# Performance work log

Measured on AMD Instinct MI355X. Metric: run time of the kernel, lower is better.

Reference implementation:

```python
import jax, jax.numpy as jnp
import numpy as np
from jax import lax

B, T, IN, H = 4096, 512, 11, 16


def lstm(x, Wih, Whh, bih, bhh):
    # x: [B, T, in]; PyTorch gate order i, f, g, o packed along 4H.
    xg = jnp.einsum('bti,gi->btg', x, Wih) + bih + bhh  # [B, T, 4H]
    h0 = jnp.zeros((x.shape[0], Whh.shape[1]), x.dtype)
    c0 = jnp.zeros_like(h0)

    def step(carry, xg_t):
        h, c = carry
        g = xg_t + h @ Whh.T                      # [B, 4H]
        i, f, gg, o = jnp.split(g, 4, axis=-1)
        i = jax.nn.sigmoid(i)
        f = jax.nn.sigmoid(f)
        gg = jnp.tanh(gg)
        o = jax.nn.sigmoid(o)
        c = f * c + i * gg
        h = o * jnp.tanh(c)
        return (h, c), h

    _, hs = lax.scan(step, (h0, c0), jnp.swapaxes(xg, 0, 1))  # hs: [T, B, H]
    return jnp.swapaxes(hs, 0, 1)  # [B, T, H]


def setup_inputs() -> dict:
    key = jax.random.key(0)
    ks = jax.random.split(key, 16)
    s = 1.0 / np.sqrt(H)
    u = lambda k, shape: jax.random.uniform(k, shape, jnp.float32, -s, s)
    return {
        'x': jax.random.normal(ks[0], (B, T, IN), jnp.float32),
        'Wih1': u(ks[1], (4 * H, IN)), 'Whh1': u(ks[2], (4 * H, H)),
        'bih1': u(ks[3], (4 * H,)), 'bhh1': u(ks[4], (4 * H,)),
        'Wih2': u(ks[5], (4 * H, H)), 'Whh2': u(ks[6], (4 * H, H)),
        'bih2': u(ks[7], (4 * H,)), 'bhh2': u(ks[8], (4 * H,)),
        'Wd1': u(ks[9], (8, H)), 'bd1': u(ks[10], (8,)),
        'Wd2': u(ks[11], (8, 8)), 'bd2': u(ks[12], (8,)),
        'Wd3': u(ks[13], (3, 8)), 'bd3': u(ks[14], (3,)),
    }


def reference(x, Wih1, Whh1, bih1, bhh1, Wih2, Whh2, bih2, bhh2,
              Wd1, bd1, Wd2, bd2, Wd3, bd3):
    h1 = lstm(x, Wih1, Whh1, bih1, bhh1)          # [B, T, H]
    # Dropout2d treated as identity (eval mode).
    h2 = lstm(h1, Wih2, Whh2, bih2, bhh2)          # [B, T, H]
    s = jax.nn.softmax(h2, axis=1)[:, -1, :]       # softmax over TIME, take last step -> [B, H]
    d = (s @ Wd1.T + bd1) @ Wd2.T + bd2
    d = d @ Wd3.T + bd3                            # [B, 3]
    return jax.nn.softmax(d, axis=1)
```

## Files before the change

### kernel.cpp

```cpp
#include <hip/hip_runtime.h>

#define T_STEPS 512
#define IN_DIM 11
#define ROW_PAD 12
#define H_DIM 16
#define ROW_F (T_STEPS * IN_DIM)
#define CHUNK_T 16
#define CHUNK_F (CHUNK_T * IN_DIM)
#define N_CHUNK (T_STEPS / CHUNK_T)
#define LOG2E 1.44269504088896340736f

typedef float v2f __attribute__((ext_vector_type(2)));
typedef float v4f __attribute__((ext_vector_type(4)));

__device__ __forceinline__ v2f pk_fma(v2f a, v2f b, v2f c) {
    v2f d;
    asm("v_pk_fma_f32 %0, %1, %2, %3" : "=v"(d) : "v"(a), "v"(b), "v"(c));
    return d;
}

template<int CTRL>
__device__ __forceinline__ float qperm(float v) {
    return __builtin_bit_cast(float,
        __builtin_amdgcn_update_dpp(0, __builtin_bit_cast(int, v),
                                    CTRL, 0xf, 0xf, true));
}

__device__ __forceinline__ float bcast_lane(float v, int l) {
    return __builtin_bit_cast(float,
        __builtin_amdgcn_readlane(__builtin_bit_cast(int, v), l));
}

__global__ __launch_bounds__(256, 4) void lstm2_head(
    const float* __restrict__ x,
    const float* __restrict__ Wih1, const float* __restrict__ Whh1,
    const float* __restrict__ bih1, const float* __restrict__ bhh1,
    const float* __restrict__ Wih2, const float* __restrict__ Whh2,
    const float* __restrict__ bih2, const float* __restrict__ bhh2,
    const float* __restrict__ Wd1, const float* __restrict__ bd1,
    const float* __restrict__ Wd2, const float* __restrict__ bd2,
    const float* __restrict__ Wd3, const float* __restrict__ bd3,
    float* __restrict__ out)
{
    __shared__ alignas(16) float xlds[2][212];
    __shared__ alignas(16) float ring[2][2][CHUNK_T][H_DIM];
    __shared__ alignas(16) float shh2[2][H_DIM];

    const int lane = threadIdx.x & 63;
    const int wid = __builtin_amdgcn_readfirstlane((int)(threadIdx.x >> 6));
    const int isL2 = wid >> 1;
    const int bw   = wid & 1;
    const int b    = blockIdx.x * 2 + bw;

    const int r   = lane >> 2;
    const int gt  = lane & 3;
    const int row = gt * H_DIM + r;

    const bool is_t = (gt == 2);
    const float M   = is_t ? (-2.0f * LOG2E) : (-LOG2E);
    const float vAa = is_t ? 2.0f : 1.0f;
    const float vBc = is_t ? -1.0f : 0.0f;

    v2f win[8], wrec[8];
    float bb;
    if (!isL2) {
        #pragma unroll
        for (int j = 0; j < 5; ++j)
            win[j] = (v2f){M * Wih1[row * IN_DIM + 2 * j],
                           M * Wih1[row * IN_DIM + 2 * j + 1]};
        win[5] = (v2f){M * Wih1[row * IN_DIM + 10], 0.0f};
        win[6] = (v2f){0.f, 0.f};
        win[7] = (v2f){0.f, 0.f};
        #pragma unroll
        for (int j = 0; j < 8; ++j)
            wrec[j] = (v2f){M * Whh1[row * H_DIM + 2 * j],
                            M * Whh1[row * H_DIM + 2 * j + 1]};
        bb = M * (bih1[row] + bhh1[row]);
    } else {
        #pragma unroll
        for (int j = 0; j < 8; ++j) {
            win[j]  = (v2f){M * Wih2[row * H_DIM + 2 * j],
                            M * Wih2[row * H_DIM + 2 * j + 1]};
            wrec[j] = (v2f){M * Whh2[row * H_DIM + 2 * j],
                            M * Whh2[row * H_DIM + 2 * j + 1]};
        }
        bb = M * (bih2[row] + bhh2[row]);
    }
    #pragma unroll
    for (int j = 0; j < 8; ++j) {
        asm volatile("" : "+v"(win[j]));
        asm volatile("" : "+v"(wrec[j]));
    }

    const int f1i = lane, f2i = lane + 64, f3i = lane + 128;
    const int p1 = (f1i / IN_DIM) * ROW_PAD + (f1i % IN_DIM);
    const int p2 = (f2i / IN_DIM) * ROW_PAD + (f2i % IN_DIM);
    const int p3 = (f3i / IN_DIM) * ROW_PAD + (f3i % IN_DIM);
    const float* __restrict__ xb = x + (size_t)b * ROW_F;

    float gl0 = 0.f, gl1 = 0.f, gl2 = 0.f;
    if (!isL2) {
        if (lane < 16) xlds[bw][lane * ROW_PAD + IN_DIM] = 0.0f;
        gl0 = xb[f1i];
        gl1 = xb[f2i];
        gl2 = xb[min(f3i, ROW_F - 1)];
    }

    float cst = 0.f, ssum = 0.f, h2v = 0.f;
    v2f hr[8];
    #pragma unroll
    for (int j = 0; j < 8; ++j) hr[j] = (v2f){0.f, 0.f};

    for (int ck = 0; ck <= N_CHUNK; ++ck) {
        __syncthreads();

        if (!isL2) {
            if (ck < N_CHUNK) {
                float* const xbuf = &xlds[bw][0];
                xbuf[p1] = gl0;
                xbuf[p2] = gl1;
                xbuf[p3] = gl2;
                if (ck + 1 < N_CHUNK) {
                    const int base = (ck + 1) * CHUNK_F;
                    gl0 = xb[base + f1i];
                    gl1 = xb[base + f2i];
                    gl2 = xb[min(base + f3i, ROW_F - 1)];
                }
                float (* const rg)[H_DIM] = ring[bw][ck & 1];
                #pragma unroll
                for (int t2 = 0; t2 < CHUNK_T; ++t2) {
                    const v2f* const xr = (const v2f*)(xbuf + t2 * ROW_PAD);
                    v2f ap = pk_fma(win[0], xr[0], (v2f){bb, 0.f});
                    v2f aq = pk_fma(win[1], xr[1], (v2f){0.f, 0.f});
                    ap = pk_fma(win[2], xr[2], ap);
                    aq = pk_fma(win[3], xr[3], aq);
                    ap = pk_fma(win[4], xr[4], ap);
                    aq = pk_fma(win[5], xr[5], aq);
                    #pragma unroll
                    for (int j = 0; j < 8; j += 2) {
                        ap = pk_fma(wrec[j],     hr[j],     ap);
                        aq = pk_fma(wrec[j + 1], hr[j + 1], aq);
                    }
                    const v2f s = ap + aq;
                    const float g = s.x + s.y;
                    const float a = __builtin_fmaf(vAa,
                        __builtin_amdgcn_rcpf(1.0f + __builtin_amdgcn_exp2f(g)), vBc);
                    const float gi = qperm<0x00>(a);
                    const float gf = qperm<0x55>(a);
                    const float gg = qperm<0xAA>(a);
                    const float go = qperm<0xFF>(a);
                    cst = __builtin_fmaf(gf, cst, gi * gg);
                    const float tc = __builtin_fmaf(2.0f,
                        __builtin_amdgcn_rcpf(1.0f +
                            __builtin_amdgcn_exp2f(-2.0f * LOG2E * cst)), -1.0f);
                    rg[t2][r] = go * tc;
                    const v4f* const hq = (const v4f*)&rg[t2][0];
                    #pragma unroll
                    for (int j = 0; j < 4; ++j) {
                        const v4f q = hq[j];
                        hr[2 * j]     = (v2f){q.x, q.y};
                        hr[2 * j + 1] = (v2f){q.z, q.w};
                    }
                }
            }
        } else {
            if (ck >= 1) {
                float (* const rg)[H_DIM] = ring[bw][(ck - 1) & 1];
                #pragma unroll
                for (int t2 = 0; t2 < CHUNK_T; ++t2) {
                    const v4f* const hq = (const v4f*)&rg[t2][0];
                    const v4f q0 = hq[0];
                    const v4f q1 = hq[1];
                    v2f ap = pk_fma(wrec[0], hr[0], (v2f){bb, 0.f});
                    v2f aq = pk_fma(wrec[1], hr[1], (v2f){0.f, 0.f});
                    #pragma unroll
                    for (int j = 2; j < 8; j += 2) {
                        ap = pk_fma(wrec[j],     hr[j],     ap);
                        aq = pk_fma(wrec[j + 1], hr[j + 1], aq);
                    }
                    ap = pk_fma(win[0], (v2f){q0.x, q0.y}, ap);
                    aq = pk_fma(win[1], (v2f){q0.z, q0.w}, aq);
                    const v4f q2 = hq[2];
                    const v4f q3 = hq[3];
                    ap = pk_fma(win[2], (v2f){q1.x, q1.y}, ap);
                    aq = pk_fma(win[3], (v2f){q1.z, q1.w}, aq);
                    ap = pk_fma(win[4], (v2f){q2.x, q2.y}, ap);
                    aq = pk_fma(win[5], (v2f){q2.z, q2.w}, aq);
                    ap = pk_fma(win[6], (v2f){q3.x, q3.y}, ap);
                    aq = pk_fma(win[7], (v2f){q3.z, q3.w}, aq);
                    const v2f s = ap + aq;
                    const float g = s.x + s.y;
                    const float a = __builtin_fmaf(vAa,
                        __builtin_amdgcn_rcpf(1.0f + __builtin_amdgcn_exp2f(g)), vBc);
                    const float gi = qperm<0x00>(a);
                    const float gf = qperm<0x55>(a);
                    const float gg = qperm<0xAA>(a);
                    const float go = qperm<0xFF>(a);
                    cst = __builtin_fmaf(gf, cst, gi * gg);
                    const float tc = __builtin_fmaf(2.0f,
                        __builtin_amdgcn_rcpf(1.0f +
                            __builtin_amdgcn_exp2f(-2.0f * LOG2E * cst)), -1.0f);
                    h2v = go * tc;
                    shh2[bw][r] = h2v;
                    const v4f* const h2q = (const v4f*)&shh2[bw][0];
                    #pragma unroll
                    for (int j = 0; j < 4; ++j) {
                        const v4f q = h2q[j];
                        hr[2 * j]     = (v2f){q.x, q.y};
                        hr[2 * j + 1] = (v2f){q.z, q.w};
                    }
                    ssum += __builtin_amdgcn_exp2f(LOG2E * h2v);
                }
            }
        }
    }

    if (isL2) {
        const float sv = __builtin_amdgcn_exp2f(LOG2E * h2v) / ssum;

        float ssb[H_DIM];
        #pragma unroll
        for (int k = 0; k < H_DIM; ++k) ssb[k] = bcast_lane(sv, 4 * k);

        const int r8 = lane & 7;
        float acc1 = bd1[r8];
        #pragma unroll
        for (int k = 0; k < H_DIM; ++k)
            acc1 = __builtin_fmaf(Wd1[r8 * H_DIM + k], ssb[k], acc1);

        float d1s[8];
        #pragma unroll
        for (int j = 0; j < 8; ++j) d1s[j] = bcast_lane(acc1, j);

        float acc2 = bd2[r8];
        #pragma unroll
        for (int k = 0; k < 8; ++k)
            acc2 = __builtin_fmaf(Wd2[r8 * 8 + k], d1s[k], acc2);

        float d2s[8];
        #pragma unroll
        for (int j = 0; j < 8; ++j) d2s[j] = bcast_lane(acc2, j);

        float lg = 0.f;
        if (lane < 3) {
            lg = bd3[lane];
            #pragma unroll
            for (int k = 0; k < 8; ++k)
                lg = __builtin_fmaf(Wd3[lane * 8 + k], d2s[k], lg);
        }
        const float l0 = bcast_lane(lg, 0);
        const float l1 = bcast_lane(lg, 1);
        const float l2 = bcast_lane(lg, 2);
        const float mx = fmaxf(l0, fmaxf(l1, l2));
        const float e0 = __builtin_amdgcn_exp2f(LOG2E * (l0 - mx));
        const float e1 = __builtin_amdgcn_exp2f(LOG2E * (l1 - mx));
        const float e2 = __builtin_amdgcn_exp2f(LOG2E * (l2 - mx));
        const float inv = 1.0f / (e0 + e1 + e2);
        if (lane < 3) {
            const float ev = (lane == 0) ? e0 : ((lane == 1) ? e1 : e2);
            out[b * 3 + lane] = ev * inv;
        }
    }
}

extern "C" void kernel_launch(void* const* d_in, const int* in_sizes, int n_in,
                              void* d_out, int out_size, void* d_ws, size_t ws_size,
                              hipStream_t stream) {
    (void)in_sizes; (void)n_in; (void)out_size; (void)d_ws; (void)ws_size;
    const float* x    = (const float*)d_in[0];
    const float* Wih1 = (const float*)d_in[1];
    const float* Whh1 = (const float*)d_in[2];
    const float* bih1 = (const float*)d_in[3];
    const float* bhh1 = (const float*)d_in[4];
    const float* Wih2 = (const float*)d_in[5];
    const float* Whh2 = (const float*)d_in[6];
    const float* bih2 = (const float*)d_in[7];
    const float* bhh2 = (const float*)d_in[8];
    const float* Wd1  = (const float*)d_in[9];
    const float* bd1  = (const float*)d_in[10];
    const float* Wd2  = (const float*)d_in[11];
    const float* bd2  = (const float*)d_in[12];
    const float* Wd3  = (const float*)d_in[13];
    const float* bd3  = (const float*)d_in[14];

    lstm2_head<<<dim3(4096 / 2), dim3(256), 0, stream>>>(
        x, Wih1, Whh1, bih1, bhh1, Wih2, Whh2, bih2, bhh2,
        Wd1, bd1, Wd2, bd2, Wd3, bd3, (float*)d_out);
}
```

Baseline: 495.2 us.

## Exchange recurrent hidden state via ds_swizzle and bpermute instead of LDS round-trip

Replaces the per-step LDS write and broadcast read of the hidden state with a distributed recurrent matvec. Each lane now holds pre-permuted Whh weights, gathers its neighbours' h values with ds_swizzle, and combines partial sums from other lane groups with ds_bpermute. The input projection is computed off the critical path and added to the recurrent result afterwards. The goal is a shorter serial dependency chain per timestep. In exchange it adds cross-lane permute latency and relies on subtle lane-index arithmetic being correct.

```diff
diff --git a/kernel.cpp b/kernel.cpp
--- a/kernel.cpp
+++ b/kernel.cpp
@@ -30,6 +30,54 @@
     return __builtin_bit_cast(float,
         __builtin_amdgcn_readlane(__builtin_bit_cast(int, v), l));
 }
+
+template<int PAT>
+__device__ __forceinline__ float swz(float v) {
+    return __builtin_bit_cast(float,
+        __builtin_amdgcn_ds_swizzle(__builtin_bit_cast(int, v), PAT));
+}
+
+__device__ __forceinline__ float bperm(int addr, float v) {
+    return __builtin_bit_cast(float,
+        __builtin_amdgcn_ds_bpermute(addr, __builtin_bit_cast(int, v)));
+}
+
+__device__ __forceinline__ float rec_dot(float hv,
+        const v2f wq0[2], const v2f wq1[2], const v2f wq2[2], const v2f wq3[2],
+        float bias, int a16, int a32, int a48) {
+    const float g1 = swz<0x101F>(hv);
+    const float g2 = swz<0x201F>(hv);
+    const float g3 = swz<0x301F>(hv);
+    const v2f hp0 = (v2f){hv, g1};
+    const v2f hp1 = (v2f){g2, g3};
+    v2f d0 = pk_fma(wq0[0], hp0, (v2f){bias, 0.f});
+    d0 = pk_fma(wq0[1], hp1, d0);
+    v2f d1 = pk_fma(wq1[0], hp0, (v2f){0.f, 0.f});
+    d1 = pk_fma(wq1[1], hp1, d1);
+    v2f d2 = pk_fma(wq2[0], hp0, (v2f){0.f, 0.f});
+    d2 = pk_fma(wq2[1], hp1, d2);
+    v2f d3 = pk_fma(wq3[0], hp0, (v2f){0.f, 0.f});
+    d3 = pk_fma(wq3[1], hp1, d3);
+    const float r1 = bperm(a16, d1.x + d1.y);
+    const float r2 = bperm(a32, d2.x + d2.y);
+    const float r3 = bperm(a48, d3.x + d3.y);
+    return (d0.x + d0.y) + r1 + r2 + r3;
+}
+
+#define ACT_STEP(gsum, cst, hv_out)                                           \
+    {                                                                         \
+        const float a_ = __builtin_fmaf(vAa,                                  \
+            __builtin_amdgcn_rcpf(1.0f + __builtin_amdgcn_exp2f(gsum)), vBc); \
+        const float gi_ = qperm<0x00>(a_);                                    \
+        const float gf_ = qperm<0x55>(a_);                                    \
+        const float gg_ = qperm<0xAA>(a_);                                    \
+        const float go_ = qperm<0xFF>(a_);                                    \
+        cst = __builtin_fmaf(gf_, cst, gi_ * gg_);                            \
+        const float tc_ = __builtin_fmaf(2.0f,                                \
+            __builtin_amdgcn_rcpf(1.0f +                                      \
+                __builtin_amdgcn_exp2f(-2.0f * LOG2E * cst)), -1.0f);         \
+        hv_out = go_ * tc_;                                                   \
+    }
 
 __global__ __launch_bounds__(256, 4) void lstm2_head(
     const float* __restrict__ x,
@@ -44,7 +92,6 @@
 {
     __shared__ alignas(16) float xlds[2][212];
     __shared__ alignas(16) float ring[2][2][CHUNK_T][H_DIM];
-    __shared__ alignas(16) float shh2[2][H_DIM];
 
     const int lane = threadIdx.x & 63;
     const int wid = __builtin_amdgcn_readfirstlane((int)(threadIdx.x >> 6));
@@ -55,13 +102,34 @@
     const int r   = lane >> 2;
     const int gt  = lane & 3;
     const int row = gt * H_DIM + r;
+    const int q     = r & 3;
+    const int rbase = r & 12;
 
     const bool is_t = (gt == 2);
     const float M   = is_t ? (-2.0f * LOG2E) : (-LOG2E);
     const float vAa = is_t ? 2.0f : 1.0f;
     const float vBc = is_t ? -1.0f : 0.0f;
 
-    v2f win[8], wrec[8];
+    const int idx0 = r;
+    const int idx1 = rbase | (q ^ 1);
+    const int idx2 = rbase | (q ^ 2);
+    const int idx3 = rbase | (q ^ 3);
+    const int rowP1 = gt * H_DIM + (r ^ 4);
+    const int rowP2 = gt * H_DIM + (r ^ 8);
+    const int rowP3 = gt * H_DIM + (r ^ 12);
+
+    const float* __restrict__ Wrec = isL2 ? Whh2 : Whh1;
+    v2f wq0[2], wq1[2], wq2[2], wq3[2];
+    wq0[0] = (v2f){M * Wrec[row  * H_DIM + idx0], M * Wrec[row  * H_DIM + idx1]};
+    wq0[1] = (v2f){M * Wrec[row  * H_DIM + idx2], M * Wrec[row  * H_DIM + idx3]};
+    wq1[0] = (v2f){M * Wrec[rowP1 * H_DIM + idx0], M * Wrec[rowP1 * H_DIM + idx1]};
+    wq1[1] = (v2f){M * Wrec[rowP1 * H_DIM + idx2], M * Wrec[rowP1 * H_DIM + idx3]};
+    wq2[0] = (v2f){M * Wrec[rowP2 * H_DIM + idx0], M * Wrec[rowP2 * H_DIM + idx1]};
+    wq2[1] = (v2f){M * Wrec[rowP2 * H_DIM + idx2], M * Wrec[rowP2 * H_DIM + idx3]};
+    wq3[0] = (v2f){M * Wrec[rowP3 * H_DIM + idx0], M * Wrec[rowP3 * H_DIM + idx1]};
+    wq3[1] = (v2f){M * Wrec[rowP3 * H_DIM + idx2], M * Wrec[rowP3 * H_DIM + idx3]};
+
+    v2f win[8];
     float bb;
     if (!isL2) {
         #pragma unroll
@@ -71,26 +139,27 @@
         win[5] = (v2f){M * Wih1[row * IN_DIM + 10], 0.0f};
         win[6] = (v2f){0.f, 0.f};
         win[7] = (v2f){0.f, 0.f};
-        #pragma unroll
-        for (int j = 0; j < 8; ++j)
-            wrec[j] = (v2f){M * Whh1[row * H_DIM + 2 * j],
-                            M * Whh1[row * H_DIM + 2 * j + 1]};
         bb = M * (bih1[row] + bhh1[row]);
     } else {
         #pragma unroll
-        for (int j = 0; j < 8; ++j) {
-            win[j]  = (v2f){M * Wih2[row * H_DIM + 2 * j],
-                            M * Wih2[row * H_DIM + 2 * j + 1]};
-            wrec[j] = (v2f){M * Whh2[row * H_DIM + 2 * j],
-                            M * Whh2[row * H_DIM + 2 * j + 1]};
-        }
+        for (int j = 0; j < 8; ++j)
+            win[j] = (v2f){M * Wih2[row * H_DIM + 2 * j],
+                           M * Wih2[row * H_DIM + 2 * j + 1]};
         bb = M * (bih2[row] + bhh2[row]);
     }
     #pragma unroll
-    for (int j = 0; j < 8; ++j) {
-        asm volatile("" : "+v"(win[j]));
-        asm volatile("" : "+v"(wrec[j]));
-    }
+    for (int j = 0; j < 8; ++j) asm volatile("" : "+v"(win[j]));
+    #pragma unroll
+    for (int j = 0; j < 2; ++j) {
+        asm volatile("" : "+v"(wq0[j]));
+        asm volatile("" : "+v"(wq1[j]));
+        asm volatile("" : "+v"(wq2[j]));
+        asm volatile("" : "+v"(wq3[j]));
+    }
+
+    const int a16 = (lane ^ 16) << 2;
+    const int a32 = (lane ^ 32) << 2;
+    const int a48 = (lane ^ 48) << 2;
 
     const int f1i = lane, f2i = lane + 64, f3i = lane + 128;
     const int p1 = (f1i / IN_DIM) * ROW_PAD + (f1i % IN_DIM);
@@ -106,10 +175,7 @@
         gl2 = xb[min(f3i, ROW_F - 1)];
     }
 
-    float cst = 0.f, ssum = 0.f, h2v = 0.f;
-    v2f hr[8];
-    #pragma unroll
-    for (int j = 0; j < 8; ++j) hr[j] = (v2f){0.f, 0.f};
+    float cst = 0.f, ssum = 0.f, hv = 0.f;
 
     for (int ck = 0; ck <= N_CHUNK; ++ck) {
         __syncthreads();
@@ -129,38 +195,18 @@
                 float (* const rg)[H_DIM] = ring[bw][ck & 1];
                 #pragma unroll
                 for (int t2 = 0; t2 < CHUNK_T; ++t2) {
+                    const float rec = rec_dot(hv, wq0, wq1, wq2, wq3, bb,
+                                              a16, a32, a48);
                     const v2f* const xr = (const v2f*)(xbuf + t2 * ROW_PAD);
-                    v2f ap = pk_fma(win[0], xr[0], (v2f){bb, 0.f});
-                    v2f aq = pk_fma(win[1], xr[1], (v2f){0.f, 0.f});
-                    ap = pk_fma(win[2], xr[2], ap);
-                    aq = pk_fma(win[3], xr[3], aq);
-                    ap = pk_fma(win[4], xr[4], ap);
-                    aq = pk_fma(win[5], xr[5], aq);
-                    #pragma unroll
-                    for (int j = 0; j < 8; j += 2) {
-                        ap = pk_fma(wrec[j],     hr[j],     ap);
-                        aq = pk_fma(wrec[j + 1], hr[j + 1], aq);
-                    }
-                    const v2f s = ap + aq;
-                    const float g = s.x + s.y;
-                    const float a = __builtin_fmaf(vAa,
-                        __builtin_amdgcn_rcpf(1.0f + __builtin_amdgcn_exp2f(g)), vBc);
-                    const float gi = qperm<0x00>(a);
-                    const float gf = qperm<0x55>(a);
-                    const float gg = qperm<0xAA>(a);
-                    const float go = qperm<0xFF>(a);
-                    cst = __builtin_fmaf(gf, cst, gi * gg);
-                    const float tc = __builtin_fmaf(2.0f,
-                        __builtin_amdgcn_rcpf(1.0f +
-                            __builtin_amdgcn_exp2f(-2.0f * LOG2E * cst)), -1.0f);
-                    rg[t2][r] = go * tc;
-                    const v4f* const hq = (const v4f*)&rg[t2][0];
-                    #pragma unroll
-                    for (int j = 0; j < 4; ++j) {
-                        const v4f q = hq[j];
-                        hr[2 * j]     = (v2f){q.x, q.y};
-                        hr[2 * j + 1] = (v2f){q.z, q.w};
-                    }
+                    v2f xa = pk_fma(win[0], xr[0], (v2f){0.f, 0.f});
+                    v2f xc = pk_fma(win[1], xr[1], (v2f){0.f, 0.f});
+                    xa = pk_fma(win[2], xr[2], xa);
+                    xc = pk_fma(win[3], xr[3], xc);
+                    xa = pk_fma(win[4], xr[4], xa);
+                    xc = pk_fma(win[5], xr[5], xc);
+                    const float g = rec + (xa.x + xa.y) + (xc.x + xc.y);
+                    ACT_STEP(g, cst, hv);
+                    rg[t2][r] = hv;
                 }
             }
         } else {
@@ -168,55 +214,31 @@
                 float (* const rg)[H_DIM] = ring[bw][(ck - 1) & 1];
                 #pragma unroll
                 for (int t2 = 0; t2 < CHUNK_T; ++t2) {
+                    const float rec = rec_dot(hv, wq0, wq1, wq2, wq3, bb,
+                                              a16, a32, a48);
                     const v4f* const hq = (const v4f*)&rg[t2][0];
                     const v4f q0 = hq[0];
                     const v4f q1 = hq[1];
-                    v2f ap = pk_fma(wrec[0], hr[0], (v2f){bb, 0.f});
-                    v2f aq = pk_fma(wrec[1], hr[1], (v2f){0.f, 0.f});
-                    #pragma unroll
-                    for (int j = 2; j < 8; j += 2) {
-                        ap = pk_fma(wrec[j],     hr[j],     ap);
-                        aq = pk_fma(wrec[j + 1], hr[j + 1], aq);
-                    }
-                    ap = pk_fma(win[0], (v2f){q0.x, q0.y}, ap);
-                    aq = pk_fma(win[1], (v2f){q0.z, q0.w}, aq);
                     const v4f q2 = hq[2];
                     const v4f q3 = hq[3];
-                    ap = pk_fma(win[2], (v2f){q1.x, q1.y}, ap);
-                    aq = pk_fma(win[3], (v2f){q1.z, q1.w}, aq);
-                    ap = pk_fma(win[4], (v2f){q2.x, q2.y}, ap);
-                    aq = pk_fma(win[5], (v2f){q2.z, q2.w}, aq);
-                    ap = pk_fma(win[6], (v2f){q3.x, q3.y}, ap);
-                    aq = pk_fma(win[7], (v2f){q3.z, q3.w}, aq);
-                    const v2f s = ap + aq;
-                    const float g = s.x + s.y;
-                    const float a = __builtin_fmaf(vAa,
-                        __builtin_amdgcn_rcpf(1.0f + __builtin_amdgcn_exp2f(g)), vBc);
-                    const float gi = qperm<0x00>(a);
-                    const float gf = qperm<0x55>(a);
-                    const float gg = qperm<0xAA>(a);
-                    const float go = qperm<0xFF>(a);
-                    cst = __builtin_fmaf(gf, cst, gi * gg);
-                    const float tc = __builtin_fmaf(2.0f,
-                        __builtin_amdgcn_rcpf(1.0f +
-                            __builtin_amdgcn_exp2f(-2.0f * LOG2E * cst)), -1.0f);
-                    h2v = go * tc;
-                    shh2[bw][r] = h2v;
-                    const v4f* const h2q = (const v4f*)&shh2[bw][0];
-                    #pragma unroll
-                    for (int j = 0; j < 4; ++j) {
-                        const v4f q = h2q[j];
-                        hr[2 * j]     = (v2f){q.x, q.y};
-                        hr[2 * j + 1] = (v2f){q.z, q.w};
-                    }
-                    ssum += __builtin_amdgcn_exp2f(LOG2E * h2v);
+                    v2f ya = pk_fma(win[0], (v2f){q0.x, q0.y}, (v2f){0.f, 0.f});
+                    v2f yc = pk_fma(win[1], (v2f){q0.z, q0.w}, (v2f){0.f, 0.f});
+                    ya = pk_fma(win[2], (v2f){q1.x, q1.y}, ya);
+                    yc = pk_fma(win[3], (v2f){q1.z, q1.w}, yc);
+                    ya = pk_fma(win[4], (v2f){q2.x, q2.y}, ya);
+                    yc = pk_fma(win[5], (v2f){q2.z, q2.w}, yc);
+                    ya = pk_fma(win[6], (v2f){q3.x, q3.y}, ya);
+                    yc = pk_fma(win[7], (v2f){q3.z, q3.w}, yc);
+                    const float g = rec + (ya.x + ya.y) + (yc.x + yc.y);
+                    ACT_STEP(g, cst, hv);
+                    ssum += __builtin_amdgcn_exp2f(LOG2E * hv);
                 }
             }
         }
     }
 
     if (isL2) {
-        const float sv = __builtin_amdgcn_exp2f(LOG2E * h2v) / ssum;
+        const float sv = __builtin_amdgcn_exp2f(LOG2E * hv) / ssum;
 
         float ssb[H_DIM];
         #pragma unroll
```

After: 540.2 us. 1.09x slower.
